# Kernel tuning notes

Hardware: AMD Instinct MI355X
Metric: run time of the kernel (lower is better)

Reference implementation:

```python
import jax, jax.numpy as jnp
import numpy as np

B, NI, NO = 32, 64, 64


def setup_inputs() -> dict:
    key = jax.random.key(0)
    k1, k2, k3, k4, k5, k6 = jax.random.split(key, 6)
    return {
        "input_re": jax.random.normal(k1, (B, NI, NI), dtype=jnp.float32),
        "input_im": jax.random.normal(k2, (B, NI, NI), dtype=jnp.float32),
        "w_re": jax.random.normal(k3, (NI, NI, NO, NO), dtype=jnp.float32),
        "w_im": jax.random.normal(k4, (NI, NI, NO, NO), dtype=jnp.float32),
        "amp_weights": jax.random.normal(k5, (NI, NI), dtype=jnp.float32),
        "phase_weights": jax.random.normal(k6, (NI, NI), dtype=jnp.float32),
    }


def reference(input_re, input_im, w_re, w_im, amp_weights, phase_weights):
    # complex input field (B, NI, NI) and diffraction kernel (NI, NI, NO, NO)
    e_in = jax.lax.complex(input_re, input_im)
    w_ip = jax.lax.complex(w_re, w_im)
    # passive transmission coefficients: sigmoid(amp) * exp(i*phase)
    ts = (jax.nn.sigmoid(amp_weights)
          * jnp.exp(1j * phase_weights.astype(jnp.complex64))).astype(jnp.complex64)
    # modulated field, then sum over input pixels (i,j) -> complex GEMM
    modulated = e_in * ts[None, :, :]                    # (B, NI, NI)
    out = jnp.einsum('bij,ijkl->bkl', modulated, w_ip)   # (B, NO, NO)
    return out
```

## Files before the change

### kernel.cpp

```cpp
#include <hip/hip_runtime.h>
#include <cstdint>
#include <cstddef>

#define KC 4096
#define NN 4096
#define NB 32
#define HALF (NB * NN)

typedef __attribute__((ext_vector_type(8))) short  bf16x8;
typedef __attribute__((ext_vector_type(16))) float f32x16;

__device__ __forceinline__ unsigned short f2bf(float f) {
    union { float f; unsigned u; } v; v.f = f;
    unsigned r = v.u + 0x7fffu + ((v.u >> 16) & 1u);
    return (unsigned short)(r >> 16);
}

__global__ __launch_bounds__(256) void prep_kernel(
    const float* __restrict__ in_re, const float* __restrict__ in_im,
    const float* __restrict__ amp,   const float* __restrict__ phase,
    uint32_t* __restrict__ wsA)
{
    int tid = blockIdx.x * 256 + threadIdx.x;
    int b = tid >> 12;
    int k = tid & (KC - 1);
    float er = in_re[tid], ei = in_im[tid];
    float a = amp[k], p = phase[k];
    float s = 1.0f / (1.0f + expf(-a));
    float sn, cs;
    sincosf(p, &sn, &cs);
    float tr = s * cs, ti = s * sn;
    float mr = er * tr - ei * ti;
    float mi = er * ti + ei * tr;
    uint32_t pk = (uint32_t)f2bf(mr) | ((uint32_t)f2bf(mi) << 16);
    wsA[((((k >> 2) << 5) + b) << 2) | (k & 3)] = pk;
}

__global__ __launch_bounds__(256) void gemm_kernel(
    const float* __restrict__ w_re, const float* __restrict__ w_im,
    const bf16x8* __restrict__ wsA, float2* __restrict__ wsP, int steps)
{
    const int lane = threadIdx.x & 63;
    const int wave = threadIdx.x >> 6;
    const int h    = lane >> 5;
    const int l32  = lane & 31;
    const int n    = blockIdx.x * 128 + wave * 32 + l32;
    const int s    = blockIdx.y;
    const int kbase = s * (steps * 8);

    f32x16 accR = {};
    f32x16 accI = {};

    const bf16x8* aptr = wsA + ((size_t)(kbase >> 2) + h) * 32 + l32;
    const float* pre = w_re + (size_t)(kbase + h * 4) * NN + n;
    const float* pim = w_im + (size_t)(kbase + h * 4) * NN + n;

#pragma unroll 4
    for (int t = 0; t < steps; ++t) {
        bf16x8 afrag = aptr[(size_t)(2 * t) * 32];
        const float* pr = pre + (size_t)t * 8 * NN;
        const float* pi = pim + (size_t)t * 8 * NN;
        float r0 = pr[0], r1 = pr[NN], r2 = pr[2 * NN], r3 = pr[3 * NN];
        float i0 = pi[0], i1 = pi[NN], i2 = pi[2 * NN], i3 = pi[3 * NN];

        bf16x8 bR, bI;
        bR[0] = (short)f2bf(r0);  bR[1] = (short)f2bf(-i0);
        bR[2] = (short)f2bf(r1);  bR[3] = (short)f2bf(-i1);
        bR[4] = (short)f2bf(r2);  bR[5] = (short)f2bf(-i2);
        bR[6] = (short)f2bf(r3);  bR[7] = (short)f2bf(-i3);
        bI[0] = (short)f2bf(i0);  bI[1] = (short)f2bf(r0);
        bI[2] = (short)f2bf(i1);  bI[3] = (short)f2bf(r1);
        bI[4] = (short)f2bf(i2);  bI[5] = (short)f2bf(r2);
        bI[6] = (short)f2bf(i3);  bI[7] = (short)f2bf(r3);

        accR = __builtin_amdgcn_mfma_f32_32x32x16_bf16(afrag, bR, accR, 0, 0, 0);
        accI = __builtin_amdgcn_mfma_f32_32x32x16_bf16(afrag, bI, accI, 0, 0, 0);
    }

#pragma unroll
    for (int r = 0; r < 16; ++r) {
        int brow = (r & 3) + 8 * (r >> 2) + 4 * h;
        float2 v; v.x = accR[r]; v.y = accI[r];
        wsP[((size_t)s * NB + brow) * NN + n] = v;
    }
}

__global__ __launch_bounds__(256) void reduce_kernel(
    const float2* __restrict__ wsP, float* __restrict__ out, int S)
{
    int tid = blockIdx.x * 256 + threadIdx.x;
    float re = 0.f, im = 0.f;
    for (int s = 0; s < S; ++s) {
        float2 v = wsP[(size_t)s * (NB * NN) + tid];
        re += v.x; im += v.y;
    }
    out[tid]        = re;
    out[HALF + tid] = im;
}

extern "C" void kernel_launch(void* const* d_in, const int* in_sizes, int n_in,
                              void* d_out, int out_size, void* d_ws, size_t ws_size,
                              hipStream_t stream)
{
    const float* in_re  = (const float*)d_in[0];
    const float* in_im  = (const float*)d_in[1];
    const float* w_re   = (const float*)d_in[2];
    const float* w_im   = (const float*)d_in[3];
    const float* amp    = (const float*)d_in[4];
    const float* phase  = (const float*)d_in[5];

    const size_t A_BYTES = (size_t)1024 * 32 * 16;
    uint32_t* wsA = (uint32_t*)d_ws;
    float2*   wsP = (float2*)((char*)d_ws + A_BYTES);

    int S = 16;
    while (S > 1 && A_BYTES + (size_t)S * NB * NN * sizeof(float2) > ws_size) S >>= 1;
    int steps = (KC / S) / 8;

    prep_kernel<<<dim3((NB * KC) / 256), dim3(256), 0, stream>>>(
        in_re, in_im, amp, phase, wsA);

    gemm_kernel<<<dim3(NN / 128, S), dim3(256), 0, stream>>>(
        w_re, w_im, (const bf16x8*)wsA, wsP, steps);

    reduce_kernel<<<dim3((NB * NN) / 256), dim3(256), 0, stream>>>(
        wsP, (float*)d_out, S);
}
```

Before: 171.6 us.

## Fuse split-K reduction into GEMM via LDS and global atomics, drop reduce kernel

The GEMM is restructured so each 512-thread block covers a 32-column strip, with its 8 waves each taking a K slice. Partial results are reduced in shared memory with atomics, then added to the output with global float atomics, and prep_kernel now zeroes the output. This removes the partial-sum workspace writes and the separate reduce kernel launch, and adds fast sin, cos and exp intrinsics plus a sign-bit flip instead of a second bf16 conversion. The costs are atomic contention, a nondeterministic summation order, and lower precision in the transcendental functions.

```diff
diff --git a/kernel.cpp b/kernel.cpp
--- a/kernel.cpp
+++ b/kernel.cpp
@@ -6,6 +6,7 @@
 #define NN 4096
 #define NB 32
 #define HALF (NB * NN)
+#define KH 4
 
 typedef __attribute__((ext_vector_type(8))) short  bf16x8;
 typedef __attribute__((ext_vector_type(16))) float f32x16;
@@ -19,34 +20,41 @@
 __global__ __launch_bounds__(256) void prep_kernel(
     const float* __restrict__ in_re, const float* __restrict__ in_im,
     const float* __restrict__ amp,   const float* __restrict__ phase,
-    uint32_t* __restrict__ wsA)
+    uint32_t* __restrict__ wsA, float* __restrict__ out)
 {
     int tid = blockIdx.x * 256 + threadIdx.x;
     int b = tid >> 12;
     int k = tid & (KC - 1);
     float er = in_re[tid], ei = in_im[tid];
     float a = amp[k], p = phase[k];
-    float s = 1.0f / (1.0f + expf(-a));
-    float sn, cs;
-    sincosf(p, &sn, &cs);
+    float s = 1.0f / (1.0f + __expf(-a));
+    float sn = __sinf(p);
+    float cs = __cosf(p);
     float tr = s * cs, ti = s * sn;
     float mr = er * tr - ei * ti;
     float mi = er * ti + ei * tr;
     uint32_t pk = (uint32_t)f2bf(mr) | ((uint32_t)f2bf(mi) << 16);
     wsA[((((k >> 2) << 5) + b) << 2) | (k & 3)] = pk;
+
+    ((float2*)out)[tid] = make_float2(0.f, 0.f);
 }
 
-__global__ __launch_bounds__(256) void gemm_kernel(
+__global__ __launch_bounds__(512, 4) void gemm_direct(
     const float* __restrict__ w_re, const float* __restrict__ w_im,
-    const bf16x8* __restrict__ wsA, float2* __restrict__ wsP, int steps)
+    const bf16x8* __restrict__ wsA, float* __restrict__ out)
 {
-    const int lane = threadIdx.x & 63;
-    const int wave = threadIdx.x >> 6;
-    const int h    = lane >> 5;
-    const int l32  = lane & 31;
-    const int n    = blockIdx.x * 128 + wave * 32 + l32;
-    const int s    = blockIdx.y;
-    const int kbase = s * (steps * 8);
+    __shared__ float accS[2][32][32];
+
+    const int tid   = threadIdx.x;
+    const int lane  = tid & 63;
+    const int wave  = tid >> 6;
+    const int h     = lane >> 5;
+    const int l32   = lane & 31;
+    const int strip = blockIdx.x;
+    const int kh    = blockIdx.y;
+    const int n     = strip * 32 + l32;
+    const int kbase = kh * (KC / KH) + wave * 128;
+    const int steps = 128 / 8;
 
     f32x16 accR = {};
     f32x16 accI = {};
@@ -63,39 +71,45 @@
         float r0 = pr[0], r1 = pr[NN], r2 = pr[2 * NN], r3 = pr[3 * NN];
         float i0 = pi[0], i1 = pi[NN], i2 = pi[2 * NN], i3 = pi[3 * NN];
 
+        unsigned short br0 = f2bf(r0), br1 = f2bf(r1), br2 = f2bf(r2), br3 = f2bf(r3);
+        unsigned short bi0 = f2bf(i0), bi1 = f2bf(i1), bi2 = f2bf(i2), bi3 = f2bf(i3);
         bf16x8 bR, bI;
-        bR[0] = (short)f2bf(r0);  bR[1] = (short)f2bf(-i0);
-        bR[2] = (short)f2bf(r1);  bR[3] = (short)f2bf(-i1);
-        bR[4] = (short)f2bf(r2);  bR[5] = (short)f2bf(-i2);
-        bR[6] = (short)f2bf(r3);  bR[7] = (short)f2bf(-i3);
-        bI[0] = (short)f2bf(i0);  bI[1] = (short)f2bf(r0);
-        bI[2] = (short)f2bf(i1);  bI[3] = (short)f2bf(r1);
-        bI[4] = (short)f2bf(i2);  bI[5] = (short)f2bf(r2);
-        bI[6] = (short)f2bf(i3);  bI[7] = (short)f2bf(r3);
+        bR[0] = (short)br0;  bR[1] = (short)(bi0 ^ 0x8000);
+        bR[2] = (short)br1;  bR[3] = (short)(bi1 ^ 0x8000);
+        bR[4] = (short)br2;  bR[5] = (short)(bi2 ^ 0x8000);
+        bR[6] = (short)br3;  bR[7] = (short)(bi3 ^ 0x8000);
+        bI[0] = (short)bi0;  bI[1] = (short)br0;
+        bI[2] = (short)bi1;  bI[3] = (short)br1;
+        bI[4] = (short)bi2;  bI[5] = (short)br2;
+        bI[6] = (short)bi3;  bI[7] = (short)br3;
 
         accR = __builtin_amdgcn_mfma_f32_32x32x16_bf16(afrag, bR, accR, 0, 0, 0);
         accI = __builtin_amdgcn_mfma_f32_32x32x16_bf16(afrag, bI, accI, 0, 0, 0);
     }
 
+    {
+        float* af = &accS[0][0][0];
+        af[tid] = 0.f; af[tid + 512] = 0.f;
+        af[tid + 1024] = 0.f; af[tid + 1536] = 0.f;
+    }
+    __syncthreads();
 #pragma unroll
     for (int r = 0; r < 16; ++r) {
         int brow = (r & 3) + 8 * (r >> 2) + 4 * h;
-        float2 v; v.x = accR[r]; v.y = accI[r];
-        wsP[((size_t)s * NB + brow) * NN + n] = v;
+        atomicAdd(&accS[0][brow][l32], accR[r]);
+        atomicAdd(&accS[1][brow][l32], accI[r]);
     }
-}
+    __syncthreads();
 
-__global__ __launch_bounds__(256) void reduce_kernel(
-    const float2* __restrict__ wsP, float* __restrict__ out, int S)
-{
-    int tid = blockIdx.x * 256 + threadIdx.x;
-    float re = 0.f, im = 0.f;
-    for (int s = 0; s < S; ++s) {
-        float2 v = wsP[(size_t)s * (NB * NN) + tid];
-        re += v.x; im += v.y;
+    {
+        const int row = tid >> 4;
+        const int c0  = (tid & 15) * 2;
+        const int nb  = strip * 32;
+        atomicAdd(&out[row * NN + nb + c0],            accS[0][row][c0]);
+        atomicAdd(&out[row * NN + nb + c0 + 1],        accS[0][row][c0 + 1]);
+        atomicAdd(&out[HALF + row * NN + nb + c0],     accS[1][row][c0]);
+        atomicAdd(&out[HALF + row * NN + nb + c0 + 1], accS[1][row][c0 + 1]);
     }
-    out[tid]        = re;
-    out[HALF + tid] = im;
 }
 
 extern "C" void kernel_launch(void* const* d_in, const int* in_sizes, int n_in,
@@ -109,20 +123,11 @@
     const float* amp    = (const float*)d_in[4];
     const float* phase  = (const float*)d_in[5];
 
-    const size_t A_BYTES = (size_t)1024 * 32 * 16;
     uint32_t* wsA = (uint32_t*)d_ws;
-    float2*   wsP = (float2*)((char*)d_ws + A_BYTES);
-
-    int S = 16;
-    while (S > 1 && A_BYTES + (size_t)S * NB * NN * sizeof(float2) > ws_size) S >>= 1;
-    int steps = (KC / S) / 8;
 
     prep_kernel<<<dim3((NB * KC) / 256), dim3(256), 0, stream>>>(
-        in_re, in_im, amp, phase, wsA);
+        in_re, in_im, amp, phase, wsA, (float*)d_out);
 
-    gemm_kernel<<<dim3(NN / 128, S), dim3(256), 0, stream>>>(
-        w_re, w_im, (const bf16x8*)wsA, wsP, steps);
-
-    reduce_kernel<<<dim3((NB * NN) / 256), dim3(256), 0, stream>>>(
-        wsP, (float*)d_out, S);
+    gemm_direct<<<dim3(NN / 32, KH), dim3(512), 0, stream>>>(
+        w_re, w_im, (const bf16x8*)wsA, (float*)d_out);
 }
```

Result: slower. 198.5 us (+15.7%).
